# Optimization experiments

Measured on AMD Instinct MI355X. Metric: run time of the kernel, lower is better.

## Reference

```python
import jax, jax.numpy as jnp
import numpy as np

THRESH = 0.5
ALPHA = 1.0
LOG_CLAMP = -100.0  # torch BCE clamps log terms at -100


def setup_inputs() -> dict:
    key = jax.random.key(0)
    kx, ky = jax.random.split(key)
    B, C, D = 2048, 2704, 5
    x = jax.random.uniform(kx, (B, C, D), dtype=jnp.float32)
    y = jax.random.uniform(ky, (B, C, D), dtype=jnp.float32)
    return {"x": x, "y": y}


def reference(x, y):
    # mask of "face" cells: label confidence > thresh
    maskf = (y[..., 0] > THRESH).astype(x.dtype)          # [B, cells]
    face_num = jnp.sum(maskf)
    bg_num = jnp.sum(1.0 - maskf)

    # MSE over box coords of positive cells (mean over face_num*4 elements)
    box_se = jnp.sum((x[..., 1:5] - y[..., 1:5]) ** 2, axis=-1)  # [B, cells]
    diff_box = jnp.sum(maskf * box_se) / (4.0 * face_num)

    # BCE on confidence channel
    c = x[..., 0]
    t = y[..., 0]
    log_c = jnp.maximum(jnp.log(c), LOG_CLAMP)
    log_1c = jnp.maximum(jnp.log1p(-c), LOG_CLAMP)
    bce = -(t * log_c + (1.0 - t) * log_1c)               # [B, cells]
    diff_c = jnp.sum(maskf * bce) / face_num

    # background BCE against target 0 -> -log(1 - c)
    diff_bg = jnp.sum((1.0 - maskf) * (-log_1c)) / bg_num

    scale = 1.0 + 1.0 / face_num
    return scale * diff_box + scale * diff_c + ALPHA * diff_bg
```

## Files before the change

kernel.cpp:

```cpp
#include <hip/hip_runtime.h>

#define N_CELLS (2048 * 2704)
#define N_QUADS (N_CELLS / 4)
#define RBLOCKS 2048
#define RTHREADS 256
#define LOG_CLAMP (-100.0f)

__global__ __launch_bounds__(RTHREADS) void mloss_partial(
    const float* __restrict__ x, const float* __restrict__ y,
    float* __restrict__ ws) {
  float cnt = 0.f, sbox = 0.f, sbce = 0.f, sbg = 0.f;

  int tid = blockIdx.x * RTHREADS + threadIdx.x;
  int stride = gridDim.x * RTHREADS;

  for (int q = tid; q < N_QUADS; q += stride) {
    const float4* xp = reinterpret_cast<const float4*>(x + (size_t)q * 20);
    const float4* yp = reinterpret_cast<const float4*>(y + (size_t)q * 20);
    float xa[20], ya[20];
#pragma unroll
    for (int k = 0; k < 5; ++k) {
      float4 v = xp[k];
      xa[4 * k + 0] = v.x; xa[4 * k + 1] = v.y;
      xa[4 * k + 2] = v.z; xa[4 * k + 3] = v.w;
    }
#pragma unroll
    for (int k = 0; k < 5; ++k) {
      float4 v = yp[k];
      ya[4 * k + 0] = v.x; ya[4 * k + 1] = v.y;
      ya[4 * k + 2] = v.z; ya[4 * k + 3] = v.w;
    }
#pragma unroll
    for (int c2 = 0; c2 < 4; ++c2) {
      const int b = 5 * c2;
      float t = ya[b];
      float c = xa[b];
      float lc  = fmaxf(__logf(c), LOG_CLAMP);
      float l1c = fmaxf(__logf(1.f - c), LOG_CLAMP);
      float d1 = xa[b + 1] - ya[b + 1];
      float d2 = xa[b + 2] - ya[b + 2];
      float d3 = xa[b + 3] - ya[b + 3];
      float d4 = xa[b + 4] - ya[b + 4];
      float se = d1 * d1 + d2 * d2 + d3 * d3 + d4 * d4;
      float bce = -(t * lc + (1.f - t) * l1c);
      bool m = (t > 0.5f);
      cnt  += m ? 1.f : 0.f;
      sbox += m ? se : 0.f;
      sbce += m ? bce : 0.f;
      sbg  += m ? 0.f : -l1c;
    }
  }

#pragma unroll
  for (int off = 32; off; off >>= 1) {
    cnt  += __shfl_down(cnt, off);
    sbox += __shfl_down(sbox, off);
    sbce += __shfl_down(sbce, off);
    sbg  += __shfl_down(sbg, off);
  }

  __shared__ float red[4][4];
  int wave = threadIdx.x >> 6;
  int lane = threadIdx.x & 63;
  if (lane == 0) {
    red[wave][0] = cnt; red[wave][1] = sbox;
    red[wave][2] = sbce; red[wave][3] = sbg;
  }
  __syncthreads();
  if (threadIdx.x == 0) {
    float r0 = 0.f, r1 = 0.f, r2 = 0.f, r3 = 0.f;
#pragma unroll
    for (int w = 0; w < 4; ++w) {
      r0 += red[w][0]; r1 += red[w][1]; r2 += red[w][2]; r3 += red[w][3];
    }
    float* o = ws + (size_t)blockIdx.x * 4;
    o[0] = r0; o[1] = r1; o[2] = r2; o[3] = r3;
  }
}

__global__ __launch_bounds__(RTHREADS) void mloss_final(
    const float* __restrict__ ws, float* __restrict__ out) {
  float r0 = 0.f, r1 = 0.f, r2 = 0.f, r3 = 0.f;
  for (int i = threadIdx.x; i < RBLOCKS; i += RTHREADS) {
    const float* p = ws + (size_t)i * 4;
    r0 += p[0]; r1 += p[1]; r2 += p[2]; r3 += p[3];
  }
#pragma unroll
  for (int off = 32; off; off >>= 1) {
    r0 += __shfl_down(r0, off);
    r1 += __shfl_down(r1, off);
    r2 += __shfl_down(r2, off);
    r3 += __shfl_down(r3, off);
  }
  __shared__ float red[4][4];
  int wave = threadIdx.x >> 6;
  int lane = threadIdx.x & 63;
  if (lane == 0) {
    red[wave][0] = r0; red[wave][1] = r1;
    red[wave][2] = r2; red[wave][3] = r3;
  }
  __syncthreads();
  if (threadIdx.x == 0) {
    float cnt = 0.f, sbox = 0.f, sbce = 0.f, sbg = 0.f;
#pragma unroll
    for (int w = 0; w < 4; ++w) {
      cnt += red[w][0]; sbox += red[w][1]; sbce += red[w][2]; sbg += red[w][3];
    }
    float face_num = cnt;
    float bg_num = (float)N_CELLS - cnt;
    float scale = 1.f + 1.f / face_num;
    out[0] = scale * (sbox / (4.f * face_num) + sbce / face_num) + sbg / bg_num;
  }
}

extern "C" void kernel_launch(void* const* d_in, const int* in_sizes, int n_in,
                              void* d_out, int out_size, void* d_ws, size_t ws_size,
                              hipStream_t stream) {
  const float* x = (const float*)d_in[0];
  const float* y = (const float*)d_in[1];
  float* ws = (float*)d_ws;
  float* out = (float*)d_out;

  mloss_partial<<<RBLOCKS, RTHREADS, 0, stream>>>(x, y, ws);
  mloss_final<<<1, RTHREADS, 0, stream>>>(ws, out);
}
```

Measured before the change: 40.31 us.

## Map each thread to one contiguous float4 for fully coalesced loads

Each thread previously loaded five strided float4s per quad of cells, so adjacent lanes touched addresses 80 bytes apart. Now each thread reads one consecutive float4 from x and y, so wavefront loads are fully contiguous. Each thread works out which cell it belongs to with T%5, and gets the mask of the previous cell's confidence through a lane shuffle, with a fallback global load for lane 0. This adds index arithmetic, selects and a log per float4 (about 25% more log work), plus one extra scattered load per wave.

```diff
diff --git a/kernel.cpp b/kernel.cpp
--- a/kernel.cpp
+++ b/kernel.cpp
@@ -1,53 +1,69 @@
 #include <hip/hip_runtime.h>
 
 #define N_CELLS (2048 * 2704)
-#define N_QUADS (N_CELLS / 4)
+#define N_ELEMS (N_CELLS * 5)
+#define N_F4    (N_ELEMS / 4)
 #define RBLOCKS 2048
 #define RTHREADS 256
+#define GSTRIDE (RBLOCKS * RTHREADS)
+#define NITER   ((N_F4 + GSTRIDE - 1) / GSTRIDE)
 #define LOG_CLAMP (-100.0f)
 
 __global__ __launch_bounds__(RTHREADS) void mloss_partial(
-    const float* __restrict__ x, const float* __restrict__ y,
-    float* __restrict__ ws) {
+    const float4* __restrict__ x4, const float4* __restrict__ y4,
+    const float* __restrict__ yflat, float* __restrict__ ws) {
   float cnt = 0.f, sbox = 0.f, sbce = 0.f, sbg = 0.f;
+  const int tid = blockIdx.x * RTHREADS + threadIdx.x;
+  const int lane = threadIdx.x & 63;
 
-  int tid = blockIdx.x * RTHREADS + threadIdx.x;
-  int stride = gridDim.x * RTHREADS;
+  for (int it = 0; it < NITER; ++it) {
+    const unsigned T = (unsigned)tid + (unsigned)it * GSTRIDE;
+    const bool act = T < (unsigned)N_F4;
 
-  for (int q = tid; q < N_QUADS; q += stride) {
-    const float4* xp = reinterpret_cast<const float4*>(x + (size_t)q * 20);
-    const float4* yp = reinterpret_cast<const float4*>(y + (size_t)q * 20);
-    float xa[20], ya[20];
+    float4 xv, yv;
+    if (act) {
+      xv = x4[T];
+      yv = y4[T];
+    } else {
+      xv = make_float4(0.5f, 0.f, 0.f, 0.f);
+      yv = make_float4(0.f, 0.f, 0.f, 0.f);
+    }
+
+    const unsigned e0 = 4u * T;
+    const unsigned r  = T % 5u;
+    const bool has_conf = (r < 4u);
+    const unsigned r0 = (r == 0u) ? 0u : (5u - r);
+
+    float tconf = (r == 0u) ? yv.x : (r == 1u) ? yv.y : (r == 2u) ? yv.z : yv.w;
+    float cconf = (r == 0u) ? xv.x : (r == 1u) ? xv.y : (r == 2u) ? xv.z : xv.w;
+    if (!has_conf) { tconf = 0.f; cconf = 0.5f; }
+
+    const float m_own_f = (tconf > 0.5f) ? 1.f : 0.f;
+
+    float m_prev_f = __shfl_up(m_own_f, 1);
+    if (lane == 0 && act && r0 != 0u) {
+      m_prev_f = (yflat[e0 - r0] > 0.5f) ? 1.f : 0.f;
+    }
+
+    {
+      float lc  = fmaxf(__logf(cconf), LOG_CLAMP);
+      float l1c = fmaxf(__logf(1.f - cconf), LOG_CLAMP);
+      float bce = -(tconf * lc + (1.f - tconf) * l1c);
+      float g = (act && has_conf) ? 1.f : 0.f;
+      cnt  += g * m_own_f;
+      sbce += g * m_own_f * bce;
+      sbg  += g * (1.f - m_own_f) * (-l1c);
+    }
+
+    const float xa[4] = {xv.x, xv.y, xv.z, xv.w};
+    const float ya[4] = {yv.x, yv.y, yv.z, yv.w};
 #pragma unroll
-    for (int k = 0; k < 5; ++k) {
-      float4 v = xp[k];
-      xa[4 * k + 0] = v.x; xa[4 * k + 1] = v.y;
-      xa[4 * k + 2] = v.z; xa[4 * k + 3] = v.w;
-    }
-#pragma unroll
-    for (int k = 0; k < 5; ++k) {
-      float4 v = yp[k];
-      ya[4 * k + 0] = v.x; ya[4 * k + 1] = v.y;
-      ya[4 * k + 2] = v.z; ya[4 * k + 3] = v.w;
-    }
-#pragma unroll
-    for (int c2 = 0; c2 < 4; ++c2) {
-      const int b = 5 * c2;
-      float t = ya[b];
-      float c = xa[b];
-      float lc  = fmaxf(__logf(c), LOG_CLAMP);
-      float l1c = fmaxf(__logf(1.f - c), LOG_CLAMP);
-      float d1 = xa[b + 1] - ya[b + 1];
-      float d2 = xa[b + 2] - ya[b + 2];
-      float d3 = xa[b + 3] - ya[b + 3];
-      float d4 = xa[b + 4] - ya[b + 4];
-      float se = d1 * d1 + d2 * d2 + d3 * d3 + d4 * d4;
-      float bce = -(t * lc + (1.f - t) * l1c);
-      bool m = (t > 0.5f);
-      cnt  += m ? 1.f : 0.f;
-      sbox += m ? se : 0.f;
-      sbce += m ? bce : 0.f;
-      sbg  += m ? 0.f : -l1c;
+    for (int j = 0; j < 4; ++j) {
+      const bool is_own = (r0 == 0u) | ((r0 + (unsigned)j) >= 5u);
+      float mask = is_own ? m_own_f : m_prev_f;
+      float isbox = (act && ((unsigned)j != r)) ? 1.f : 0.f;
+      float d = xa[j] - ya[j];
+      sbox += isbox * mask * d * d;
     }
   }
 
@@ -61,20 +77,19 @@
 
   __shared__ float red[4][4];
   int wave = threadIdx.x >> 6;
-  int lane = threadIdx.x & 63;
-  if (lane == 0) {
+  if ((threadIdx.x & 63) == 0) {
     red[wave][0] = cnt; red[wave][1] = sbox;
     red[wave][2] = sbce; red[wave][3] = sbg;
   }
   __syncthreads();
   if (threadIdx.x == 0) {
-    float r0 = 0.f, r1 = 0.f, r2 = 0.f, r3 = 0.f;
+    float r0s = 0.f, r1s = 0.f, r2s = 0.f, r3s = 0.f;
 #pragma unroll
     for (int w = 0; w < 4; ++w) {
-      r0 += red[w][0]; r1 += red[w][1]; r2 += red[w][2]; r3 += red[w][3];
+      r0s += red[w][0]; r1s += red[w][1]; r2s += red[w][2]; r3s += red[w][3];
     }
     float* o = ws + (size_t)blockIdx.x * 4;
-    o[0] = r0; o[1] = r1; o[2] = r2; o[3] = r3;
+    o[0] = r0s; o[1] = r1s; o[2] = r2s; o[3] = r3s;
   }
 }
 
@@ -94,8 +109,7 @@
   }
   __shared__ float red[4][4];
   int wave = threadIdx.x >> 6;
-  int lane = threadIdx.x & 63;
-  if (lane == 0) {
+  if ((threadIdx.x & 63) == 0) {
     red[wave][0] = r0; red[wave][1] = r1;
     red[wave][2] = r2; red[wave][3] = r3;
   }
@@ -121,6 +135,7 @@
   float* ws = (float*)d_ws;
   float* out = (float*)d_out;
 
-  mloss_partial<<<RBLOCKS, RTHREADS, 0, stream>>>(x, y, ws);
+  mloss_partial<<<RBLOCKS, RTHREADS, 0, stream>>>(
+      (const float4*)x, (const float4*)y, y, ws);
   mloss_final<<<1, RTHREADS, 0, stream>>>(ws, out);
 }
```

New measurement: 43.95 us. 1.09x slower.
